# Performance work log

Hardware: AMD Instinct MI355X
Metric: run time of the kernel (lower is better)

Reference implementation:

```python
import jax, jax.numpy as jnp
import numpy as np

# Mamba2 defaults (mamba_ssm): expand=2, headdim=64, d_conv=4, ngroups=1
D_MODEL, D_STATE, D_INNER, HEADDIM, D_CONV = 512, 64, 1024, 64, 4
NHEADS = D_INNER // HEADDIM  # 16
CONV_DIM = D_INNER + 2 * D_STATE  # 1152
D_IN_PROJ = 2 * D_INNER + 2 * D_STATE + NHEADS  # 2192
BATCH, SEQLEN = 2, 2048
RMS_EPS = 1.1920929e-07  # torch nn.RMSNorm eps=None -> fp32 machine eps
GNORM_EPS = 1e-5  # mamba_ssm RMSNormGated default


def _rms(t, w, eps):
    return t * jax.lax.rsqrt(jnp.mean(t * t, axis=-1, keepdims=True) + eps) * w


def _mamba2(u, in_w, conv_w, conv_b, dt_bias, A_log, Dp, gnorm_w, out_w):
    """Mamba2 block forward (ngroups=1). u: (b, l, d_model) -> (b, l, d_model)."""
    b, l, _ = u.shape
    zxbcdt = jnp.einsum('bld,ed->ble', u, in_w)  # (b, l, 2192)
    z = zxbcdt[..., :D_INNER]
    xBC = zxbcdt[..., D_INNER:D_INNER + CONV_DIM]
    dt = jax.nn.softplus(zxbcdt[..., -NHEADS:] + dt_bias)  # (b, l, h)
    # causal depthwise conv, kernel D_CONV, then SiLU
    xp = jnp.pad(xBC, ((0, 0), (D_CONV - 1, 0), (0, 0)))
    xBC = conv_b + sum(xp[:, i:i + l, :] * conv_w[:, i] for i in range(D_CONV))
    xBC = jax.nn.silu(xBC)
    x = xBC[..., :D_INNER].reshape(b, l, NHEADS, HEADDIM)
    Bm = xBC[..., D_INNER:D_INNER + D_STATE]  # (b, l, n)
    Cm = xBC[..., D_INNER + D_STATE:]         # (b, l, n)
    dA = jnp.exp(dt * (-jnp.exp(A_log)))      # (b, l, h), decay per head

    def step(h, inp):
        dA_t, dt_t, B_t, C_t, x_t = inp  # (b,h) (b,h) (b,n) (b,n) (b,h,p)
        h = h * dA_t[:, :, None, None] + jnp.einsum('bh,bhp,bn->bhpn', dt_t, x_t, B_t)
        y = jnp.einsum('bhpn,bn->bhp', h, C_t)
        return h, y

    h0 = jnp.zeros((b, NHEADS, HEADDIM, D_STATE), u.dtype)
    xs = (jnp.swapaxes(dA, 0, 1), jnp.swapaxes(dt, 0, 1), jnp.swapaxes(Bm, 0, 1),
          jnp.swapaxes(Cm, 0, 1), jnp.swapaxes(x, 0, 1))
    _, ys = jax.lax.scan(step, h0, xs)  # (l, b, h, p)
    y = jnp.swapaxes(ys, 0, 1) + x * Dp[None, None, :, None]
    y = y.reshape(b, l, D_INNER)
    # gated RMSNorm: norm(y * silu(z)) * weight
    y = y * jax.nn.silu(z)
    y = _rms(y, gnorm_w, GNORM_EPS)
    return jnp.einsum('bli,oi->blo', y, out_w)


def _layer(x, pos_emb, pixel_mask, norm_ssm_w, norm_ffn_w, ffn_w1, ffn_b1, ffn_w2, ffn_b2,
           f_in_w, f_conv_w, f_conv_b, f_dt_bias, f_A_log, f_D, f_gnorm_w, f_out_w,
           b_in_w, b_conv_w, b_conv_b, b_dt_bias, b_A_log, b_D, b_gnorm_w, b_out_w):
    si = _rms(x, norm_ssm_w, RMS_EPS) + pos_emb
    fwd = _mamba2(si, f_in_w, f_conv_w, f_conv_b, f_dt_bias, f_A_log, f_D, f_gnorm_w, f_out_w)
    bwd = jnp.flip(_mamba2(jnp.flip(si, 1), b_in_w, b_conv_w, b_conv_b, b_dt_bias,
                           b_A_log, b_D, b_gnorm_w, b_out_w), 1)
    ssm_out = (fwd + bwd) * pixel_mask[..., None]  # merge='add'
    x = x + ssm_out
    h = _rms(x, norm_ffn_w, RMS_EPS)
    h = jax.nn.gelu(h @ ffn_w1.T + ffn_b1, approximate=False)
    return x + (h @ ffn_w2.T + ffn_b2)


def setup_inputs() -> dict:
    key = jax.random.key(0)
    ks = jax.random.split(key, 16)
    f32 = jnp.float32
    inp = {}
    inp['x'] = jax.random.normal(ks[0], (BATCH, SEQLEN, D_MODEL), f32)
    inp['pos_emb'] = jax.random.normal(ks[1], (BATCH, SEQLEN, D_MODEL), f32) * 0.02
    inp['pixel_mask'] = jnp.ones((BATCH, SEQLEN), f32)
    inp['norm_ssm_w'] = jnp.ones((D_MODEL,), f32)
    inp['norm_ffn_w'] = jnp.ones((D_MODEL,), f32)
    d_ffn = 4 * D_MODEL
    inp['ffn_w1'] = jax.random.normal(ks[2], (d_ffn, D_MODEL), f32) * 0.02
    inp['ffn_b1'] = jnp.zeros((d_ffn,), f32)
    inp['ffn_w2'] = jax.random.normal(ks[3], (D_MODEL, d_ffn), f32) * 0.02
    inp['ffn_b2'] = jnp.zeros((D_MODEL,), f32)
    i = 4
    for pre in ('f', 'b'):
        inp[pre + '_in_w'] = jax.random.normal(ks[i], (D_IN_PROJ, D_MODEL), f32) * 0.02; i += 1
        inp[pre + '_conv_w'] = jax.random.uniform(ks[i], (CONV_DIM, D_CONV), f32, -0.5, 0.5); i += 1
        inp[pre + '_conv_b'] = jnp.zeros((CONV_DIM,), f32)
        dt0 = jnp.exp(jax.random.uniform(ks[i], (NHEADS,), f32) * (jnp.log(0.1) - jnp.log(0.001)) + jnp.log(0.001)); i += 1
        inp[pre + '_dt_bias'] = dt0 + jnp.log(-jnp.expm1(-dt0))  # inverse softplus
        inp[pre + '_A_log'] = jnp.log(jax.random.uniform(ks[i], (NHEADS,), f32, 1.0, 16.0)); i += 1
        inp[pre + '_D'] = jnp.ones((NHEADS,), f32)
        inp[pre + '_gnorm_w'] = jnp.ones((D_INNER,), f32)
        inp[pre + '_out_w'] = jax.random.normal(ks[i], (D_MODEL, D_INNER), f32) * 0.02; i += 1
    return inp


def reference(x, pos_emb, pixel_mask, norm_ssm_w, norm_ffn_w, ffn_w1, ffn_b1, ffn_w2, ffn_b2,
              f_in_w, f_conv_w, f_conv_b, f_dt_bias, f_A_log, f_D, f_gnorm_w, f_out_w,
              b_in_w, b_conv_w, b_conv_b, b_dt_bias, b_A_log, b_D, b_gnorm_w, b_out_w):
    return _layer(x, pos_emb, pixel_mask, norm_ssm_w, norm_ffn_w, ffn_w1, ffn_b1, ffn_w2, ffn_b2,
                  f_in_w, f_conv_w, f_conv_b, f_dt_bias, f_A_log, f_D, f_gnorm_w, f_out_w,
                  b_in_w, b_conv_w, b_conv_b, b_dt_bias, b_A_log, b_D, b_gnorm_w, b_out_w)
```

## Files before the change

kernel.cpp:

```cpp
#include <hip/hip_runtime.h>
#include <hip/hip_bf16.h>

typedef unsigned short u16;
typedef unsigned int u32;
typedef __bf16 bf16x8 __attribute__((ext_vector_type(8)));
typedef float f32x4 __attribute__((ext_vector_type(4)));

typedef __attribute__((address_space(1))) void gvoid_t;
typedef __attribute__((address_space(3))) void lvoid_t;
__device__ __forceinline__ void lds_cp16(void* lds, const void* g) {
    __builtin_amdgcn_global_load_lds((gvoid_t*)g, (lvoid_t*)lds, 16, 0, 0);
}

__device__ __forceinline__ float bf2f(u16 v) {
    u32 x = (u32)v << 16;
    return __builtin_bit_cast(float, x);
}
__device__ __forceinline__ u16 f2bf(float f) {
    return __builtin_bit_cast(u16, (__bf16)f);
}

__device__ __forceinline__ float block_sum_256(float v, float* red) {
    #pragma unroll
    for (int o = 32; o > 0; o >>= 1) v += __shfl_xor(v, o);
    int w = threadIdx.x >> 6;
    if ((threadIdx.x & 63) == 0) red[w] = v;
    __syncthreads();
    return red[0] + red[1] + red[2] + red[3];
}

__global__ __launch_bounds__(256) void k_prep(
    const float* __restrict__ f_inw, const float* __restrict__ b_inw,
    const float* __restrict__ f_ow, const float* __restrict__ b_ow,
    const float* __restrict__ w1, const float* __restrict__ w2,
    u16* __restrict__ INWF, u16* __restrict__ INWB,
    u16* __restrict__ OWF, u16* __restrict__ OWB,
    u16* __restrict__ W1B, u16* __restrict__ W2B,
    const float* __restrict__ x, const float* __restrict__ pe,
    const float* __restrict__ wrms, u16* __restrict__ sib) {
    if (blockIdx.x < 21504) {
        int i = blockIdx.x * 256 + threadIdx.x;
        if (i < 1179648) { int n = i >> 9; INWF[i] = (n < 2192) ? f2bf(f_inw[i]) : (u16)0; return; }
        i -= 1179648;
        if (i < 1179648) { int n = i >> 9; INWB[i] = (n < 2192) ? f2bf(b_inw[i]) : (u16)0; return; }
        i -= 1179648;
        if (i < 524288) { OWF[i] = f2bf(f_ow[i]); return; }
        i -= 524288;
        if (i < 524288) { OWB[i] = f2bf(b_ow[i]); return; }
        i -= 524288;
        if (i < 1048576) { W1B[i] = f2bf(w1[i]); return; }
        i -= 1048576;
        if (i < 1048576) W2B[i] = f2bf(w2[i]);
        return;
    }
    __shared__ float red[4];
    int row = blockIdx.x - 21504, t = threadIdx.x;
    size_t base = (size_t)row * 512 + t * 2;
    float2 xv = *(const float2*)(x + base);
    float ss = block_sum_256(xv.x * xv.x + xv.y * xv.y, red);
    float sc = rsqrtf(ss * (1.f / 512.f) + 1.1920929e-07f);
    float2 pv = *(const float2*)(pe + base);
    float2 wv = *(const float2*)(wrms + t * 2);
    sib[base] = f2bf(xv.x * sc * wv.x + pv.x);
    sib[base + 1] = f2bf(xv.y * sc * wv.y + pv.y);
}

__global__ __launch_bounds__(256) void k_gemm_in(
    const u16* __restrict__ A, const u16* __restrict__ W0, const u16* __restrict__ W1,
    u16* __restrict__ Z0, u16* __restrict__ Z1,
    u16* __restrict__ XB0, u16* __restrict__ XB1) {
    const int z = blockIdx.z;
    const u16* W = z ? W1 : W0;
    u16* Z = z ? Z1 : Z0;
    u16* XB = z ? XB1 : XB0;
    const int K = 512;

    __shared__ __align__(16) u16 As[128 * 64];
    __shared__ __align__(16) u16 Bs[128 * 64];

    const int t = threadIdx.x;
    const int lane = t & 63;
    const int w = t >> 6;
    const int m0 = blockIdx.y * 128;
    const int n0 = blockIdx.x * 128;
    const int wm = (w >> 1) * 64;
    const int wn = (w & 1) * 64;
    const int fr = lane & 15;
    const int fk = (lane >> 4) * 8;

    f32x4 acc[4][4];
    #pragma unroll
    for (int i = 0; i < 4; ++i)
        #pragma unroll
        for (int j = 0; j < 4; ++j) acc[i][j] = (f32x4){0.f, 0.f, 0.f, 0.f};

    for (int kt = 0; kt < K; kt += 64) {
        #pragma unroll
        for (int j = 0; j < 4; ++j) {
            int off16 = j * 256 + t;
            int row = off16 >> 3;
            int kc = (off16 & 7) * 8;
            int gm = m0 + row;
            if (z) gm = (gm & ~2047) | (2047 - (gm & 2047));
            lds_cp16(As + off16 * 8, A + (size_t)gm * K + kt + kc);
            lds_cp16(Bs + off16 * 8, W + (size_t)(n0 + row) * K + kt + kc);
        }
        __syncthreads();
        #pragma unroll
        for (int k0 = 0; k0 < 64; k0 += 32) {
            bf16x8 af[4], bfr[4];
            #pragma unroll
            for (int i = 0; i < 4; ++i) af[i] = *(const bf16x8*)(As + (wm + i * 16 + fr) * 64 + k0 + fk);
            #pragma unroll
            for (int i = 0; i < 4; ++i) bfr[i] = *(const bf16x8*)(Bs + (wn + i * 16 + fr) * 64 + k0 + fk);
            #pragma unroll
            for (int i = 0; i < 4; ++i)
                #pragma unroll
                for (int j = 0; j < 4; ++j)
                    acc[i][j] = __builtin_amdgcn_mfma_f32_16x16x32_bf16(af[i], bfr[j], acc[i][j], 0, 0, 0);
        }
        __syncthreads();
    }
    #pragma unroll
    for (int i = 0; i < 4; ++i) {
        int rbase = m0 + wm + i * 16 + (lane >> 4) * 4;
        #pragma unroll
        for (int j = 0; j < 4; ++j) {
            int c = n0 + wn + j * 16 + fr;
            #pragma unroll
            for (int r = 0; r < 4; ++r) {
                u16 v = f2bf(acc[i][j][r]);
                int m = rbase + r;
                if (c < 1024) Z[(size_t)m * 1024 + c] = v;
                else if (c < 2192) XB[(size_t)m * 1184 + (c - 1024)] = v;
            }
        }
    }
}

template <int EPI>
__global__ __launch_bounds__(256) void k_gemm64(
    const u16* __restrict__ A0, const u16* __restrict__ A1,
    const u16* __restrict__ W0, const u16* __restrict__ W1,
    u16* __restrict__ C0, u16* __restrict__ C1, int N, int K,
    const float* __restrict__ bias, float* __restrict__ outf) {
    const int z = blockIdx.z;
    const u16* A = (EPI == 3) ? A0 : (z ? A1 : A0);
    const u16* W = (EPI == 3) ? W0 : (z ? W1 : W0);
    u16* C = z ? C1 : C0;
    int kbeg = 0, kend = K;
    if (EPI == 3) { kbeg = z * (K >> 1); kend = kbeg + (K >> 1); }

    __shared__ __align__(16) u16 As[64 * 32];
    __shared__ __align__(16) u16 Bs[64 * 32];

    const int t = threadIdx.x;
    const int lane = t & 63;
    const int w = t >> 6;
    const int m0 = blockIdx.y * 64;
    const int n0 = blockIdx.x * 64;
    const int wm = (w >> 1) * 32;
    const int wn = (w & 1) * 32;
    const int fr = lane & 15;
    const int fk = (lane >> 4) * 8;

    f32x4 acc[2][2];
    #pragma unroll
    for (int i = 0; i < 2; ++i)
        #pragma unroll
        for (int j = 0; j < 2; ++j) acc[i][j] = (f32x4){0.f, 0.f, 0.f, 0.f};

    const int srow = t >> 2;
    const int skc = (t & 3) * 8;
    for (int kt = kbeg; kt < kend; kt += 32) {
        lds_cp16(As + t * 8, A + (size_t)(m0 + srow) * K + kt + skc);
        lds_cp16(Bs + t * 8, W + (size_t)(n0 + srow) * K + kt + skc);
        __syncthreads();
        bf16x8 af[2], bfr[2];
        #pragma unroll
        for (int i = 0; i < 2; ++i) af[i] = *(const bf16x8*)(As + (wm + i * 16 + fr) * 32 + fk);
        #pragma unroll
        for (int j = 0; j < 2; ++j) bfr[j] = *(const bf16x8*)(Bs + (wn + j * 16 + fr) * 32 + fk);
        #pragma unroll
        for (int i = 0; i < 2; ++i)
            #pragma unroll
            for (int j = 0; j < 2; ++j)
                acc[i][j] = __builtin_amdgcn_mfma_f32_16x16x32_bf16(af[i], bfr[j], acc[i][j], 0, 0, 0);
        __syncthreads();
    }
    #pragma unroll
    for (int i = 0; i < 2; ++i) {
        int rbase = m0 + wm + i * 16 + (lane >> 4) * 4;
        #pragma unroll
        for (int j = 0; j < 2; ++j) {
            int col = n0 + wn + j * 16 + fr;
            #pragma unroll
            for (int r = 0; r < 4; ++r) {
                int m = rbase + r;
                float v = acc[i][j][r];
                if (EPI == 0) {
                    C[(size_t)m * N + col] = f2bf(v);
                } else if (EPI == 1) {
                    float xg = v + bias[col];
                    C[(size_t)m * N + col] = f2bf(0.5f * xg * (1.f + erff(xg * 0.70710678118654752f)));
                } else {
                    atomicAdd(outf + (size_t)m * N + col, v);
                }
            }
        }
    }
}

__global__ __launch_bounds__(160) void k_conv(
    const u16* __restrict__ xb0, const u16* __restrict__ xb1,
    const float* __restrict__ cw0, const float* __restrict__ cb0,
    const float* __restrict__ dtb0, const float* __restrict__ al0,
    const float* __restrict__ cw1, const float* __restrict__ cb1,
    const float* __restrict__ dtb1, const float* __restrict__ al1,
    u16* __restrict__ xc0, u16* __restrict__ xc1,
    float* __restrict__ dtO0, float* __restrict__ dAO0,
    float* __restrict__ dtO1, float* __restrict__ dAO1) {
    int g = blockIdx.x;
    int dir = g >> 9;
    int row0 = (g & 511) * 8;
    const u16* xb = dir ? xb1 : xb0;
    const float* cw = dir ? cw1 : cw0;
    const float* cb = dir ? cb1 : cb0;
    const float* dtb = dir ? dtb1 : dtb0;
    const float* al = dir ? al1 : al0;
    u16* xc = dir ? xc1 : xc0;
    float* dtO = dir ? dtO1 : dtO0;
    float* dAO = dir ? dAO1 : dAO0;
    int tl0 = row0 & 2047;
    int rbatch = row0 - tl0;
    int t = threadIdx.x;
    if (t < 144) {
        int col = t * 8;
        float cwa[8][4];
        #pragma unroll
        for (int j = 0; j < 8; ++j) {
            float4 c4 = *(const float4*)(cw + (col + j) * 4);
            cwa[j][0] = c4.x; cwa[j][1] = c4.y; cwa[j][2] = c4.z; cwa[j][3] = c4.w;
        }
        float cbv[8];
        float4 cb0v = *(const float4*)(cb + col);
        float4 cb1v = *(const float4*)(cb + col + 4);
        cbv[0] = cb0v.x; cbv[1] = cb0v.y; cbv[2] = cb0v.z; cbv[3] = cb0v.w;
        cbv[4] = cb1v.x; cbv[5] = cb1v.y; cbv[6] = cb1v.z; cbv[7] = cb1v.w;
        uint4 win[4];
        win[0] = win[1] = win[2] = make_uint4(0, 0, 0, 0);
        #pragma unroll
        for (int i = 0; i < 3; ++i) {
            int tt = tl0 - 3 + i;
            if (tt >= 0) win[i] = *(const uint4*)(xb + (size_t)(rbatch + tt) * 1184 + col);
        }
        for (int s = 0; s < 8; ++s) {
            win[3] = *(const uint4*)(xb + (size_t)(rbatch + tl0 + s) * 1184 + col);
            const u16* w0 = (const u16*)&win[0];
            const u16* w1 = (const u16*)&win[1];
            const u16* w2 = (const u16*)&win[2];
            const u16* w3 = (const u16*)&win[3];
            u16 ov[8];
            #pragma unroll
            for (int j = 0; j < 8; ++j) {
                float a = cbv[j] + bf2f(w0[j]) * cwa[j][0] + bf2f(w1[j]) * cwa[j][1]
                        + bf2f(w2[j]) * cwa[j][2] + bf2f(w3[j]) * cwa[j][3];
                ov[j] = f2bf(a / (1.f + expf(-a)));
            }
            *(uint4*)(xc + (size_t)(row0 + s) * 1152 + col) = *(const uint4*)ov;
            win[0] = win[1]; win[1] = win[2]; win[2] = win[3];
        }
    } else if (t < 160) {
        int hh = t - 144;
        float nal = -expf(al[hh]);
        float dtbv = dtb[hh];
        for (int s = 0; s < 8; ++s) {
            int row = row0 + s;
            float v = bf2f(xb[(size_t)row * 1184 + 1152 + hh]) + dtbv;
            float sp = (v > 20.f) ? v : log1pf(expf(v));
            dtO[row * 16 + hh] = sp;
            dAO[row * 16 + hh] = nal * sp;
        }
    }
}

__global__ __launch_bounds__(256) void k_ssd_state(
    const u16* __restrict__ xc0, const float* __restrict__ dt0, const float* __restrict__ ld0,
    const u16* __restrict__ xc1, const float* __restrict__ dt1, const float* __restrict__ ld1,
    float* __restrict__ S, float* __restrict__ Aprod) {
    int blk = blockIdx.x;
    int c = blk & 31, h = (blk >> 5) & 15, b = (blk >> 9) & 1, dir = blk >> 10;
    const u16* xc = dir ? xc1 : xc0;
    const float* dtp = dir ? dt1 : dt0;
    const float* ldp = dir ? ld1 : ld0;
    const int t = threadIdx.x, w = t >> 6, lane = t & 63;
    const int fr = lane & 15, fk = (lane >> 4) * 8;

    __shared__ __align__(16) u16 sBt[64 * 72];
    __shared__ __align__(16) u16 sXp[64 * 72];
    __shared__ float ssc[64];
    size_t row0 = (size_t)b * 2048 + c * 64;

    if (t < 64) {
        float v = ldp[(row0 + t) * 16 + h];
        float dtv = dtp[(row0 + t) * 16 + h];
        #pragma unroll
        for (int o = 1; o < 64; o <<= 1) {
            float u = __shfl_up(v, o);
            if (lane >= o) v += u;
        }
        float last = __shfl(v, 63);
        ssc[t] = dtv * expf(last - v);
        if (t == 63) Aprod[blk] = expf(v);
    }
    __syncthreads();
    #pragma unroll
    for (int i2 = t; i2 < 512; i2 += 256) {
        int r = i2 >> 3, e8 = (i2 & 7) * 8;
        size_t rb = (row0 + r) * 1152;
        uint4 bv = *(const uint4*)(xc + rb + 1024 + e8);
        uint4 xv = *(const uint4*)(xc + rb + h * 64 + e8);
        const u16* bs = (const u16*)&bv;
        const u16* xs = (const u16*)&xv;
        float sc = ssc[r];
        #pragma unroll
        for (int j = 0; j < 8; ++j) {
            sBt[(e8 + j) * 72 + r] = bs[j];
            sXp[(e8 + j) * 72 + r] = f2bf(bf2f(xs[j]) * sc);
        }
    }
    __syncthreads();

    f32x4 acc[4];
    #pragma unroll
    for (int j = 0; j < 4; ++j) acc[j] = (f32x4){0.f, 0.f, 0.f, 0.f};
    #pragma unroll
    for (int k0 = 0; k0 < 64; k0 += 32) {
        bf16x8 a = *(const bf16x8*)(sBt + (w * 16 + fr) * 72 + k0 + fk);
        #pragma unroll
        for (int j = 0; j < 4; ++j) {
            bf16x8 bb = *(const bf16x8*)(sXp + (j * 16 + fr) * 72 + k0 + fk);
            acc[j] = __builtin_amdgcn_mfma_f32_16x16x32_bf16(a, bb, acc[j], 0, 0, 0);
        }
    }
    float* Sb = S + (size_t)blk * 4096;
    int nb = w * 16 + (lane >> 4) * 4;
    #pragma unroll
    for (int j = 0; j < 4; ++j) {
        int p = j * 16 + fr;
        *(f32x4*)(Sb + p * 64 + nb) = acc[j];
    }
}

__global__ __launch_bounds__(256) void k_scan_carry(float* __restrict__ S,
                                                    const float* __restrict__ Aprod) {
    int g = blockIdx.x;
    int blk = g >> 4;
    int e = (g & 15) * 256 + threadIdx.x;
    size_t base = (size_t)blk * 32 * 4096 + e;
    float sv[32];
    #pragma unroll
    for (int c = 0; c < 32; ++c) sv[c] = S[base + (size_t)c * 4096];
    float ap[32];
    #pragma unroll
    for (int c = 0; c < 32; ++c) ap[c] = Aprod[blk * 32 + c];
    float h = 0.f;
    #pragma unroll
    for (int c = 0; c < 32; ++c) {
        S[base + (size_t)c * 4096] = h;
        h = ap[c] * h + sv[c];
    }
}

__global__ __launch_bounds__(256) void k_ssd_y(
    const u16* __restrict__ xc0, const float* __restrict__ dt0, const float* __restrict__ ld0,
    const float* __restrict__ Dv0, u16* __restrict__ y0,
    const u16* __restrict__ xc1, const float* __restrict__ dt1, const float* __restrict__ ld1,
    const float* __restrict__ Dv1, u16* __restrict__ y1,
    const float* __restrict__ S) {
    int blk = blockIdx.x;
    int c = blk & 31, h = (blk >> 5) & 15, b = (blk >> 9) & 1, dir = blk >> 10;
    const u16* xc = dir ? xc1 : xc0;
    const float* dtp = dir ? dt1 : dt0;
    const float* ldp = dir ? ld1 : ld0;
    u16* y = dir ? y1 : y0;
    const float Dh = (dir ? Dv1 : Dv0)[h];
    const int t = threadIdx.x, w = t >> 6, lane = t & 63;
    const int fr = lane & 15, fk = (lane >> 4) * 8;

    __shared__ __align__(16) u16 sB[64 * 72];
    __shared__ __align__(16) u16 sC[64 * 72];
    __shared__ __align__(16) u16 sXp[64 * 72];
    __shared__ __align__(16) u16 sHi[64 * 72];
    __shared__ __align__(16) u16 sLo[64 * 72];
    __shared__ __align__(16) u16 sGl[64 * 72];
    __shared__ float scl[64], sdt[64];
    size_t row0 = (size_t)b * 2048 + c * 64;

    if (t < 64) {
        float v = ldp[(row0 + t) * 16 + h];
        float dtv = dtp[(row0 + t) * 16 + h];
        #pragma unroll
        for (int o = 1; o < 64; o <<= 1) {
            float u = __shfl_up(v, o);
            if (lane >= o) v += u;
        }
        scl[t] = v;
        sdt[t] = dtv;
    }
    __syncthreads();
    #pragma unroll
    for (int i2 = t; i2 < 512; i2 += 256) {
        int r = i2 >> 3, e8 = (i2 & 7) * 8;
        size_t rb = (row0 + r) * 1152;
        *(uint4*)(sB + r * 72 + e8) = *(const uint4*)(xc + rb + 1024 + e8);
        *(uint4*)(sC + r * 72 + e8) = *(const uint4*)(xc + rb + 1088 + e8);
        uint4 xv = *(const uint4*)(xc + rb + h * 64 + e8);
        const u16* xs = (const u16*)&xv;
        float dtv = sdt[r];
        #pragma unroll
        for (int j = 0; j < 8; ++j) sXp[(e8 + j) * 72 + r] = f2bf(bf2f(xs[j]) * dtv);
    }
    #pragma unroll
    for (int i4 = t; i4 < 1024; i4 += 256) {
        int p = i4 >> 4, n4 = (i4 & 15) * 4;
        float4 hv = *(const float4*)(S + (size_t)blk * 4096 + p * 64 + n4);
        ushort4 hi4, lo4;
        hi4.x = f2bf(hv.x); lo4.x = f2bf(hv.x - bf2f(hi4.x));
        hi4.y = f2bf(hv.y); lo4.y = f2bf(hv.y - bf2f(hi4.y));
        hi4.z = f2bf(hv.z); lo4.z = f2bf(hv.z - bf2f(hi4.z));
        hi4.w = f2bf(hv.w); lo4.w = f2bf(hv.w - bf2f(hi4.w));
        *(ushort4*)(sHi + p * 72 + n4) = hi4;
        *(ushort4*)(sLo + p * 72 + n4) = lo4;
    }
    __syncthreads();

    f32x4 g[4], acc2[4];
    #pragma unroll
    for (int j = 0; j < 4; ++j) { g[j] = (f32x4){0.f,0.f,0.f,0.f}; acc2[j] = (f32x4){0.f,0.f,0.f,0.f}; }
    #pragma unroll
    for (int k0 = 0; k0 < 64; k0 += 32) {
        bf16x8 a = *(const bf16x8*)(sC + (w * 16 + fr) * 72 + k0 + fk);
        #pragma unroll
        for (int j = 0; j < 4; ++j) {
            bf16x8 bb = *(const bf16x8*)(sB + (j * 16 + fr) * 72 + k0 + fk);
            g[j] = __builtin_amdgcn_mfma_f32_16x16x32_bf16(a, bb, g[j], 0, 0, 0);
            bf16x8 bh = *(const bf16x8*)(sHi + (j * 16 + fr) * 72 + k0 + fk);
            acc2[j] = __builtin_amdgcn_mfma_f32_16x16x32_bf16(a, bh, acc2[j], 0, 0, 0);
            bf16x8 bl = *(const bf16x8*)(sLo + (j * 16 + fr) * 72 + k0 + fk);
            acc2[j] = __builtin_amdgcn_mfma_f32_16x16x32_bf16(a, bl, acc2[j], 0, 0, 0);
        }
    }
    #pragma unroll
    for (int j = 0; j < 4; ++j) {
        int r = j * 16 + fr;
        #pragma unroll
        for (int reg = 0; reg < 4; ++reg) {
            int s = w * 16 + (lane >> 4) * 4 + reg;
            float val = (r <= s) ? expf(scl[s] - scl[r]) * g[j][reg] : 0.f;
            sGl[s * 72 + r] = f2bf(val);
        }
    }
    __syncthreads();

    f32x4 acc1[4];
    #pragma unroll
    for (int j = 0; j < 4; ++j) acc1[j] = (f32x4){0.f, 0.f, 0.f, 0.f};
    #pragma unroll
    for (int k0 = 0; k0 < 64; k0 += 32) {
        bf16x8 a = *(const bf16x8*)(sGl + (w * 16 + fr) * 72 + k0 + fk);
        #pragma unroll
        for (int j = 0; j < 4; ++j) {
            bf16x8 bb = *(const bf16x8*)(sXp + (j * 16 + fr) * 72 + k0 + fk);
            acc1[j] = __builtin_amdgcn_mfma_f32_16x16x32_bf16(a, bb, acc1[j], 0, 0, 0);
        }
    }
    #pragma unroll
    for (int reg = 0; reg < 4; ++reg) {
        int s = w * 16 + (lane >> 4) * 4 + reg;
        float es = expf(scl[s]);
        size_t yrb = (row0 + s) * 1024 + h * 64;
        size_t xrb = (row0 + s) * 1152 + h * 64;
        #pragma unroll
        for (int j = 0; j < 4; ++j) {
            int p = j * 16 + fr;
            float xv = bf2f(xc[xrb + p]);
            y[yrb + p] = f2bf(acc1[j][reg] + es * acc2[j][reg] + xv * Dh);
        }
    }
}

__global__ __launch_bounds__(256) void k_gnorm(
    const u16* __restrict__ y0, const u16* __restrict__ z0,
    const float* __restrict__ gw0, u16* __restrict__ o0,
    const u16* __restrict__ y1, const u16* __restrict__ z1,
    const float* __restrict__ gw1, u16* __restrict__ o1) {
    __shared__ float red[4];
    int r = blockIdx.x;
    int dir = r >> 12, row = r & 4095;
    int t = threadIdx.x;
    const u16* y = dir ? y1 : y0;
    const u16* zp = dir ? z1 : z0;
    const float* gw = dir ? gw1 : gw0;
    u16* o = dir ? o1 : o0;
    ushort4 yv = *(const ushort4*)(y + (size_t)row * 1024 + t * 4);
    ushort4 zr = *(const ushort4*)(zp + (size_t)row * 1024 + t * 4);
    float z0f = bf2f(zr.x), z1f = bf2f(zr.y), z2f = bf2f(zr.z), z3f = bf2f(zr.w);
    float v0 = bf2f(yv.x) * (z0f / (1.f + expf(-z0f)));
    float v1 = bf2f(yv.y) * (z1f / (1.f + expf(-z1f)));
    float v2 = bf2f(yv.z) * (z2f / (1.f + expf(-z2f)));
    float v3 = bf2f(yv.w) * (z3f / (1.f + expf(-z3f)));
    float ss = block_sum_256(v0 * v0 + v1 * v1 + v2 * v2 + v3 * v3, red);
    float sc = rsqrtf(ss * (1.f / 1024.f) + 1e-5f);
    float4 gv = *(const float4*)(gw + t * 4);
    size_t ob = (size_t)row * 1024 + t * 4;
    o[ob + 0] = f2bf(v0 * sc * gv.x);
    o[ob + 1] = f2bf(v1 * sc * gv.y);
    o[ob + 2] = f2bf(v2 * sc * gv.z);
    o[ob + 3] = f2bf(v3 * sc * gv.w);
}

__global__ __launch_bounds__(256) void k_add_rms(
    const float* __restrict__ x, const u16* __restrict__ of,
    const u16* __restrict__ ob, const float* __restrict__ mask,
    const float* __restrict__ wrms, const float* __restrict__ b2,
    float* __restrict__ x2, u16* __restrict__ o, float* __restrict__ outf) {
    __shared__ float red[4];
    int row = blockIdx.x, t = threadIdx.x;
    int bb = row >> 11, tl = row & 2047;
    size_t fb = (size_t)((bb << 11) + (2047 - tl)) * 512;
    float m = mask[row];
    size_t base = (size_t)row * 512 + t * 2;
    size_t fo = fb + t * 2;
    float2 xv = *(const float2*)(x + base);
    float v0 = xv.x + (bf2f(of[base]) + bf2f(ob[fo])) * m;
    float v1 = xv.y + (bf2f(of[base + 1]) + bf2f(ob[fo + 1])) * m;
    x2[base] = v0;
    x2[base + 1] = v1;
    float2 b2v = *(const float2*)(b2 + t * 2);
    outf[base] = v0 + b2v.x;
    outf[base + 1] = v1 + b2v.y;
    float ss = block_sum_256(v0 * v0 + v1 * v1, red);
    float sc = rsqrtf(ss * (1.f / 512.f) + 1.1920929e-07f);
    float2 wv = *(const float2*)(wrms + t * 2);
    o[base] = f2bf(v0 * sc * wv.x);
    o[base + 1] = f2bf(v1 * sc * wv.y);
}

extern "C" void kernel_launch(void* const* d_in, const int* in_sizes, int n_in,
                              void* d_out, int out_size, void* d_ws, size_t ws_size,
                              hipStream_t stream) {
    const float* x = (const float*)d_in[0];
    const float* pe = (const float*)d_in[1];
    const float* mask = (const float*)d_in[2];
    const float* nsw = (const float*)d_in[3];
    const float* nfw = (const float*)d_in[4];
    const float* w1 = (const float*)d_in[5];
    const float* b1 = (const float*)d_in[6];
    const float* w2 = (const float*)d_in[7];
    const float* b2 = (const float*)d_in[8];
    const float* f_inw = (const float*)d_in[9];
    const float* f_cw = (const float*)d_in[10];
    const float* f_cb = (const float*)d_in[11];
    const float* f_dtb = (const float*)d_in[12];
    const float* f_al = (const float*)d_in[13];
    const float* f_D = (const float*)d_in[14];
    const float* f_gw = (const float*)d_in[15];
    const float* f_ow = (const float*)d_in[16];
    const float* b_inw = (const float*)d_in[17];
    const float* b_cw = (const float*)d_in[18];
    const float* b_cb = (const float*)d_in[19];
    const float* b_dtb = (const float*)d_in[20];
    const float* b_al = (const float*)d_in[21];
    const float* b_D = (const float*)d_in[22];
    const float* b_gw = (const float*)d_in[23];
    const float* b_ow = (const float*)d_in[24];
    float* out = (float*)d_out;

    char* ws = (char*)d_ws;
    u16* Z0   = (u16*)(ws + 0);
    u16* Z1   = (u16*)(ws + 8388608);
    u16* XB0  = (u16*)(ws + 16777216);
    u16* XB1  = (u16*)(ws + 26476544);
    u16* INWF = (u16*)(ws + 36175872);
    u16* INWB = (u16*)(ws + 38535168);
    u16* SIB  = (u16*)(ws + 40894464);
    u16* XC0  = (u16*)(ws + 36175872);
    u16* XC1  = (u16*)(ws + 45613056);
    float* dtF = (float*)(ws + 55050240);
    float* dAF = (float*)(ws + 55312384);
    float* dtB = (float*)(ws + 55574528);
    float* dAB = (float*)(ws + 55836672);
    u16* Y0   = (u16*)(ws + 16777216);
    u16* Y1   = (u16*)(ws + 25165824);
    u16* YG0  = (u16*)(ws + 36175872);
    u16* YG1  = (u16*)(ws + 44564480);
    u16* OP0  = (u16*)(ws + 0);
    u16* OP1  = (u16*)(ws + 4194304);
    float* X2 = (float*)(ws + 8388608);
    u16* X2B  = (u16*)(ws + 0);
    u16* HACT = (u16*)(ws + 16777216);
    u16* OWF = (u16*)(ws + 56098816);
    u16* OWB = (u16*)(ws + 57147392);
    u16* W1B = (u16*)(ws + 58195968);
    u16* W2B = (u16*)(ws + 60293120);
    float* SBUF = (float*)(ws + 62390272);
    float* APR  = (float*)(ws + 95944704);

    k_prep<<<25600, 256, 0, stream>>>(f_inw, b_inw, f_ow, b_ow, w1, w2,
                                      INWF, INWB, OWF, OWB, W1B, W2B,
                                      x, pe, nsw, SIB);
    k_gemm_in<<<dim3(18, 32, 2), 256, 0, stream>>>(SIB, INWF, INWB, Z0, Z1, XB0, XB1);
    k_conv<<<1024, 160, 0, stream>>>(XB0, XB1, f_cw, f_cb, f_dtb, f_al,
                                     b_cw, b_cb, b_dtb, b_al,
                                     XC0, XC1, dtF, dAF, dtB, dAB);
    k_ssd_state<<<2048, 256, 0, stream>>>(XC0, dtF, dAF, XC1, dtB, dAB, SBUF, APR);
    k_scan_carry<<<1024, 256, 0, stream>>>(SBUF, APR);
    k_ssd_y<<<2048, 256, 0, stream>>>(XC0, dtF, dAF, f_D, Y0,
                                      XC1, dtB, dAB, b_D, Y1, SBUF);
    k_gnorm<<<8192, 256, 0, stream>>>(Y0, Z0, f_gw, YG0, Y1, Z1, b_gw, YG1);
    k_gemm64<0><<<dim3(8, 64, 2), 256, 0, stream>>>(YG0, YG1, OWF, OWB, OP0, OP1, 512, 1024,
                                                    nullptr, nullptr);
    k_add_rms<<<4096, 256, 0, stream>>>(x, OP0, OP1, mask, nfw, b2, X2, X2B, out);
    k_gemm64<1><<<dim3(32, 64, 1), 256, 0, stream>>>(X2B, X2B, W1B, W1B, HACT, HACT, 2048, 512,
                                                     b1, nullptr);
    k_gemm64<3><<<dim3(8, 64, 2), 256, 0, stream>>>(HACT, HACT, W2B, W2B, nullptr, nullptr,
                                                    512, 2048, nullptr, out);
}
```

Before: 344.3 us.

## Replace split-K atomic FFN down-proj with direct epilogue fusing bias and residual

The FFN second GEMM no longer splits K across two z-slices with atomicAdd into the output. It now runs a single pass that writes bias plus residual plus accumulator directly, so the residual-plus-bias write moves out of the add-RMS kernel. This removes atomic traffic and the output pre-initialisation, at the cost of half as many blocks for the long-K GEMM. Separately, the input-projection GEMM K-tile is halved from 64 to 32, which shrinks LDS use, possibly improving occupancy, but doubles the number of barriers.

```diff
diff --git a/kernel.cpp b/kernel.cpp
--- a/kernel.cpp
+++ b/kernel.cpp
@@ -75,8 +75,8 @@
     u16* XB = z ? XB1 : XB0;
     const int K = 512;
 
-    __shared__ __align__(16) u16 As[128 * 64];
-    __shared__ __align__(16) u16 Bs[128 * 64];
+    __shared__ __align__(16) u16 As[128 * 32];
+    __shared__ __align__(16) u16 Bs[128 * 32];
 
     const int t = threadIdx.x;
     const int lane = t & 63;
@@ -94,31 +94,28 @@
         #pragma unroll
         for (int j = 0; j < 4; ++j) acc[i][j] = (f32x4){0.f, 0.f, 0.f, 0.f};
 
-    for (int kt = 0; kt < K; kt += 64) {
-        #pragma unroll
-        for (int j = 0; j < 4; ++j) {
+    for (int kt = 0; kt < K; kt += 32) {
+        #pragma unroll
+        for (int j = 0; j < 2; ++j) {
             int off16 = j * 256 + t;
-            int row = off16 >> 3;
-            int kc = (off16 & 7) * 8;
+            int row = off16 >> 2;
+            int kc = (off16 & 3) * 8;
             int gm = m0 + row;
             if (z) gm = (gm & ~2047) | (2047 - (gm & 2047));
             lds_cp16(As + off16 * 8, A + (size_t)gm * K + kt + kc);
             lds_cp16(Bs + off16 * 8, W + (size_t)(n0 + row) * K + kt + kc);
         }
         __syncthreads();
-        #pragma unroll
-        for (int k0 = 0; k0 < 64; k0 += 32) {
-            bf16x8 af[4], bfr[4];
+        bf16x8 af[4], bfr[4];
+        #pragma unroll
+        for (int i = 0; i < 4; ++i) af[i] = *(const bf16x8*)(As + (wm + i * 16 + fr) * 32 + fk);
+        #pragma unroll
+        for (int i = 0; i < 4; ++i) bfr[i] = *(const bf16x8*)(Bs + (wn + i * 16 + fr) * 32 + fk);
+        #pragma unroll
+        for (int i = 0; i < 4; ++i)
             #pragma unroll
-            for (int i = 0; i < 4; ++i) af[i] = *(const bf16x8*)(As + (wm + i * 16 + fr) * 64 + k0 + fk);
-            #pragma unroll
-            for (int i = 0; i < 4; ++i) bfr[i] = *(const bf16x8*)(Bs + (wn + i * 16 + fr) * 64 + k0 + fk);
-            #pragma unroll
-            for (int i = 0; i < 4; ++i)
-                #pragma unroll
-                for (int j = 0; j < 4; ++j)
-                    acc[i][j] = __builtin_amdgcn_mfma_f32_16x16x32_bf16(af[i], bfr[j], acc[i][j], 0, 0, 0);
-        }
+            for (int j = 0; j < 4; ++j)
+                acc[i][j] = __builtin_amdgcn_mfma_f32_16x16x32_bf16(af[i], bfr[j], acc[i][j], 0, 0, 0);
         __syncthreads();
     }
     #pragma unroll
@@ -143,13 +140,12 @@
     const u16* __restrict__ A0, const u16* __restrict__ A1,
     const u16* __restrict__ W0, const u16* __restrict__ W1,
     u16* __restrict__ C0, u16* __restrict__ C1, int N, int K,
-    const float* __restrict__ bias, float* __restrict__ outf) {
+    const float* __restrict__ bias, const float* __restrict__ resid,
+    float* __restrict__ outf) {
     const int z = blockIdx.z;
-    const u16* A = (EPI == 3) ? A0 : (z ? A1 : A0);
-    const u16* W = (EPI == 3) ? W0 : (z ? W1 : W0);
+    const u16* A = z ? A1 : A0;
+    const u16* W = z ? W1 : W0;
     u16* C = z ? C1 : C0;
-    int kbeg = 0, kend = K;
-    if (EPI == 3) { kbeg = z * (K >> 1); kend = kbeg + (K >> 1); }
 
     __shared__ __align__(16) u16 As[64 * 32];
     __shared__ __align__(16) u16 Bs[64 * 32];
@@ -172,7 +168,7 @@
 
     const int srow = t >> 2;
     const int skc = (t & 3) * 8;
-    for (int kt = kbeg; kt < kend; kt += 32) {
+    for (int kt = 0; kt < K; kt += 32) {
         lds_cp16(As + t * 8, A + (size_t)(m0 + srow) * K + kt + skc);
         lds_cp16(Bs + t * 8, W + (size_t)(n0 + srow) * K + kt + skc);
         __syncthreads();
@@ -204,7 +200,7 @@
                     float xg = v + bias[col];
                     C[(size_t)m * N + col] = f2bf(0.5f * xg * (1.f + erff(xg * 0.70710678118654752f)));
                 } else {
-                    atomicAdd(outf + (size_t)m * N + col, v);
+                    outf[(size_t)m * N + col] = v + bias[col] + resid[(size_t)m * N + col];
                 }
             }
         }
@@ -523,8 +519,8 @@
 __global__ __launch_bounds__(256) void k_add_rms(
     const float* __restrict__ x, const u16* __restrict__ of,
     const u16* __restrict__ ob, const float* __restrict__ mask,
-    const float* __restrict__ wrms, const float* __restrict__ b2,
-    float* __restrict__ x2, u16* __restrict__ o, float* __restrict__ outf) {
+    const float* __restrict__ wrms,
+    float* __restrict__ x2, u16* __restrict__ o) {
     __shared__ float red[4];
     int row = blockIdx.x, t = threadIdx.x;
     int bb = row >> 11, tl = row & 2047;
@@ -537,9 +533,6 @@
     float v1 = xv.y + (bf2f(of[base + 1]) + bf2f(ob[fo + 1])) * m;
     x2[base] = v0;
     x2[base + 1] = v1;
-    float2 b2v = *(const float2*)(b2 + t * 2);
-    outf[base] = v0 + b2v.x;
-    outf[base + 1] = v1 + b2v.y;
     float ss = block_sum_256(v0 * v0 + v1 * v1, red);
     float sc = rsqrtf(ss * (1.f / 512.f) + 1.1920929e-07f);
     float2 wv = *(const float2*)(wrms + t * 2);
@@ -620,10 +613,10 @@
                                       XC1, dtB, dAB, b_D, Y1, SBUF);
     k_gnorm<<<8192, 256, 0, stream>>>(Y0, Z0, f_gw, YG0, Y1, Z1, b_gw, YG1);
     k_gemm64<0><<<dim3(8, 64, 2), 256, 0, stream>>>(YG0, YG1, OWF, OWB, OP0, OP1, 512, 1024,
-                                                    nullptr, nullptr);
-    k_add_rms<<<4096, 256, 0, stream>>>(x, OP0, OP1, mask, nfw, b2, X2, X2B, out);
+                                                    nullptr, nullptr, nullptr);
+    k_add_rms<<<4096, 256, 0, stream>>>(x, OP0, OP1, mask, nfw, X2, X2B);
     k_gemm64<1><<<dim3(32, 64, 1), 256, 0, stream>>>(X2B, X2B, W1B, W1B, HACT, HACT, 2048, 512,
-                                                     b1, nullptr);
-    k_gemm64<3><<<dim3(8, 64, 2), 256, 0, stream>>>(HACT, HACT, W2B, W2B, nullptr, nullptr,
-                                                    512, 2048, nullptr, out);
-}
+                                                     b1, nullptr, nullptr);
+    k_gemm64<2><<<dim3(8, 64, 1), 256, 0, stream>>>(HACT, HACT, W2B, W2B, nullptr, nullptr,
+                                                    512, 2048, b2, X2, out);
+}
```

Measured after the change: 331.5 us. 1.04x faster.
